# Kernel optimization log

Measured on AMD Instinct MI355X. Metric: run time of the kernel, lower is better.

Reference implementation:

```python
import jax, jax.numpy as jnp
import numpy as np

ALPHA = 0.2
NEG = -9e15
EPS = 1e-5


def _gat(h, adj, W, a, out_features):
    # h: [B,N,Fin], adj: [B,N,N], W: [Fin,Fout], a: [2*Fout,1]
    Wh = jnp.matmul(h, W)                      # [B,N,Fout]
    Wh1 = jnp.matmul(Wh, a[:out_features])     # [B,N,1]
    Wh2 = jnp.matmul(Wh, a[out_features:])     # [B,N,1]
    e = Wh1 + jnp.swapaxes(Wh2, 1, 2)          # [B,N,N]
    e = jax.nn.leaky_relu(e, negative_slope=ALPHA)
    scores = jnp.where(adj > 0, e, NEG)
    att = jax.nn.softmax(scores, axis=1)       # NOTE: dim=1 as in source
    return jnp.matmul(att, Wh)                 # [B,N,Fout]


def _layernorm(x, g, b):
    mu = jnp.mean(x, axis=-1, keepdims=True)
    var = jnp.var(x, axis=-1, keepdims=True)
    return (x - mu) * jax.lax.rsqrt(var + EPS) * g + b


def setup_inputs() -> dict:
    key = jax.random.key(0)
    ks = jax.random.split(key, 8)
    B, N, F, H = 2, 4096, 256, 1024
    x = jax.random.normal(ks[0], (B, N, F), dtype=jnp.float32)
    adj = jax.random.randint(ks[1], (B, N, N), 0, 2, dtype=jnp.int32)
    def xavier(k, shape):
        fan_in, fan_out = shape[0], shape[1]
        lim = np.sqrt(6.0 / (fan_in + fan_out))
        return jax.random.uniform(k, shape, jnp.float32, -lim, lim)
    return {
        "x": x,
        "adj": adj,
        "W1": xavier(ks[2], (F, F)),
        "a1": xavier(ks[3], (2 * F, 1)),
        "W2": xavier(ks[4], (F, F)),
        "a2": xavier(ks[5], (2 * F, 1)),
        "w_ff1": xavier(ks[6], (F, H)) ,
        "b_ff1": jnp.zeros((H,), jnp.float32),
        "w_ff2": xavier(ks[7], (H, F)),
        "b_ff2": jnp.zeros((F,), jnp.float32),
        "g_ln1": jnp.ones((F,), jnp.float32),
        "b_ln1": jnp.zeros((F,), jnp.float32),
        "g_ln2": jnp.ones((F,), jnp.float32),
        "b_ln2": jnp.zeros((F,), jnp.float32),
    }


def reference(x, adj, W1, a1, W2, a2, w_ff1, b_ff1, w_ff2, b_ff2,
              g_ln1, b_ln1, g_ln2, b_ln2):
    Fout = W1.shape[1]
    residual = x
    # dropout is a no-op in eval mode
    h = _gat(x, adj, W1, a1, Fout)          # single head -> cat is identity
    h = _gat(h, adj, W2, a2, W2.shape[1])
    h = _layernorm(residual + h, g_ln1, b_ln1)
    residual2 = h
    ff = jnp.matmul(jax.nn.relu(jnp.matmul(h, w_ff1) + b_ff1), w_ff2) + b_ff2
    return _layernorm(residual2 + ff, g_ln2, b_ln2)
```

## Files before the change

kernel.cpp:

```cpp
#include <hip/hip_runtime.h>
#include <math.h>

#define ALPHA 0.2f
#define NEGV  -9e15f
#define EPSV  1e-5f

constexpr int B_ = 2, N_ = 4096, F_ = 256, H_ = 1024;
constexpr int SPLIT_ = 16;
constexpr int SPLITJ_ = 4;

typedef __attribute__((ext_vector_type(4))) float f32x4;
typedef __attribute__((ext_vector_type(8))) short s16x8;

__device__ __forceinline__ unsigned short f2bf(float f) {
    unsigned u = __builtin_bit_cast(unsigned, f);
    u += 0x7fffu + ((u >> 16) & 1u);
    return (unsigned short)(u >> 16);
}

__global__ __launch_bounds__(256) void transp_all_kernel(
    const float* __restrict__ W1, const float* __restrict__ W2,
    const float* __restrict__ F1s, const float* __restrict__ F2s,
    unsigned short* __restrict__ D1, unsigned short* __restrict__ D2,
    unsigned short* __restrict__ D3, unsigned short* __restrict__ D4,
    float* __restrict__ Zp)
{
    const int mi = blockIdx.z;
    const float* src; unsigned short* dst; int R, Cc;
    if (mi == 0)      { src = W1;  dst = D1; R = 256;  Cc = 256; }
    else if (mi == 1) { src = W2;  dst = D2; R = 256;  Cc = 256; }
    else if (mi == 2) { src = F1s; dst = D3; R = 256;  Cc = 1024; }
    else              { src = F2s; dst = D4; R = 1024; Cc = 256; }
    const int r0 = blockIdx.x * 64, c0 = blockIdx.y * 64;
    const int t = threadIdx.x;

    if (mi == 0 && blockIdx.y >= 4) {
        const int lid = (blockIdx.y - 4) * 16 + blockIdx.x;
        if (lid < 32) {
            const int i = (lid * 256 + t) * 4;
            *(float4*)&Zp[i] = make_float4(0.f, 0.f, 0.f, 0.f);
        }
        return;
    }
    if (r0 >= R || c0 >= Cc) return;

    __shared__ float T[64][65];
    #pragma unroll
    for (int s = 0; s < 4; ++s) {
        const int rr = s * 16 + (t >> 4);
        const int cq = t & 15;
        const float4 v = *(const float4*)&src[(size_t)(r0 + rr) * Cc + c0 + cq * 4];
        T[rr][cq * 4 + 0] = v.x; T[rr][cq * 4 + 1] = v.y;
        T[rr][cq * 4 + 2] = v.z; T[rr][cq * 4 + 3] = v.w;
    }
    __syncthreads();
    #pragma unroll
    for (int s = 0; s < 4; ++s) {
        const int cr = s * 16 + (t >> 4);
        const int rq = t & 15;
        ushort4 o;
        o.x = f2bf(T[rq * 4 + 0][cr]);
        o.y = f2bf(T[rq * 4 + 1][cr]);
        o.z = f2bf(T[rq * 4 + 2][cr]);
        o.w = f2bf(T[rq * 4 + 3][cr]);
        *(ushort4*)&dst[(size_t)(c0 + cr) * R + r0 + rq * 4] = o;
    }
}

__global__ __launch_bounds__(256) void gemm128_kernel(
    const void* __restrict__ Ap, const unsigned short* __restrict__ Wt,
    const float* __restrict__ bias, void* __restrict__ Cp,
    unsigned short* __restrict__ Tout, const float* __restrict__ wha,
    float* __restrict__ Wh1, float* __restrict__ Wh2,
    int Nc, int K, int relu, int a_bf16, int c_mode)
{
    __shared__ unsigned short As[128 * 72];
    __shared__ unsigned short Bs[128 * 72];
    const int t = threadIdx.x;
    const int w = t >> 6, l = t & 63;
    const int quad = l >> 4, l15 = l & 15;
    const int wr = w & 1, wc = w >> 1;
    const int row0 = blockIdx.y * 128, col0 = blockIdx.x * 128;
    const int sr = t >> 1;
    const int sk = (t & 1) * 32;

    f32x4 acc[4][4];
    #pragma unroll
    for (int it = 0; it < 4; ++it)
        #pragma unroll
        for (int ft = 0; ft < 4; ++ft) acc[it][ft] = (f32x4)(0.f);

    for (int k0 = 0; k0 < K; k0 += 64) {
        if (a_bf16) {
            const unsigned short* ap =
                (const unsigned short*)Ap + (size_t)(row0 + sr) * K + k0 + sk;
            #pragma unroll
            for (int u = 0; u < 4; ++u)
                *(s16x8*)&As[sr * 72 + sk + u * 8] = *(const s16x8*)(ap + u * 8);
        } else {
            const float* ap = (const float*)Ap + (size_t)(row0 + sr) * K + k0 + sk;
            #pragma unroll
            for (int u = 0; u < 8; ++u) {
                const float4 v = *(const float4*)(ap + u * 4);
                ushort4 o;
                o.x = f2bf(v.x); o.y = f2bf(v.y); o.z = f2bf(v.z); o.w = f2bf(v.w);
                *(ushort4*)&As[sr * 72 + sk + u * 4] = o;
            }
        }
        {
            const unsigned short* bp = Wt + (size_t)(col0 + sr) * K + k0 + sk;
            #pragma unroll
            for (int u = 0; u < 4; ++u)
                *(s16x8*)&Bs[sr * 72 + sk + u * 8] = *(const s16x8*)(bp + u * 8);
        }
        __syncthreads();
        #pragma unroll
        for (int ks = 0; ks < 64; ks += 32) {
            s16x8 af[4], bf[4];
            #pragma unroll
            for (int it = 0; it < 4; ++it)
                af[it] = *(const s16x8*)&As[(wr * 64 + it * 16 + l15) * 72 + ks + quad * 8];
            #pragma unroll
            for (int ft = 0; ft < 4; ++ft)
                bf[ft] = *(const s16x8*)&Bs[(wc * 64 + ft * 16 + l15) * 72 + ks + quad * 8];
            #pragma unroll
            for (int ft = 0; ft < 4; ++ft)
                #pragma unroll
                for (int it = 0; it < 4; ++it)
                    acc[it][ft] = __builtin_amdgcn_mfma_f32_16x16x32_bf16(
                        af[it], bf[ft], acc[it][ft], 0, 0, 0);
        }
        __syncthreads();
    }

    if (c_mode) {
        #pragma unroll
        for (int ft = 0; ft < 4; ++ft) {
            const int col = col0 + wc * 64 + ft * 16 + l15;
            const float bv = bias ? bias[col] : 0.f;
            #pragma unroll
            for (int it = 0; it < 4; ++it) {
                const int rbase = row0 + wr * 64 + it * 16 + quad * 4;
                #pragma unroll
                for (int rr = 0; rr < 4; ++rr) {
                    float v = acc[it][ft][rr] + bv;
                    if (relu) v = fmaxf(v, 0.f);
                    if (c_mode == 2)
                        ((unsigned short*)Cp)[(size_t)(rbase + rr) * Nc + col] = f2bf(v);
                    else
                        ((float*)Cp)[(size_t)(rbase + rr) * Nc + col] = v;
                }
            }
        }
    }

    if (Tout) {
        const int bb = row0 >> 12;
        #pragma unroll
        for (int ft = 0; ft < 4; ++ft) {
            const int col = col0 + wc * 64 + ft * 16 + l15;
            #pragma unroll
            for (int it = 0; it < 4; ++it) {
                const int ibase = (row0 & (N_ - 1)) + wr * 64 + it * 16 + quad * 4;
                ushort4 o;
                o.x = f2bf(acc[it][ft][0]); o.y = f2bf(acc[it][ft][1]);
                o.z = f2bf(acc[it][ft][2]); o.w = f2bf(acc[it][ft][3]);
                *(ushort4*)&Tout[((size_t)bb * F_ + col) * N_ + ibase] = o;
            }
        }
    }

    if (wha) {
        float a1v[4], a2v[4];
        #pragma unroll
        for (int ft = 0; ft < 4; ++ft) {
            const int col = col0 + wc * 64 + ft * 16 + l15;
            a1v[ft] = wha[col];
            a2v[ft] = wha[F_ + col];
        }
        #pragma unroll
        for (int it = 0; it < 4; ++it)
            #pragma unroll
            for (int rr = 0; rr < 4; ++rr) {
                float s1 = 0.f, s2 = 0.f;
                #pragma unroll
                for (int ft = 0; ft < 4; ++ft) {
                    s1 += acc[it][ft][rr] * a1v[ft];
                    s2 += acc[it][ft][rr] * a2v[ft];
                }
                #pragma unroll
                for (int mkk = 1; mkk < 16; mkk <<= 1) {
                    s1 += __shfl_xor(s1, mkk);
                    s2 += __shfl_xor(s2, mkk);
                }
                if (l15 == 0) {
                    const int row = row0 + wr * 64 + it * 16 + quad * 4 + rr;
                    atomicAdd(&Wh1[row], s1);
                    atomicAdd(&Wh2[row], s2);
                }
            }
    }
}

__global__ __launch_bounds__(256) void gemm64_kernel(
    const void* __restrict__ Ap, const unsigned short* __restrict__ Wt,
    const float* __restrict__ bias, void* __restrict__ Cp,
    unsigned short* __restrict__ Tout, const float* __restrict__ wha,
    float* __restrict__ Wh1, float* __restrict__ Wh2,
    int Nc, int K, int relu, int a_mode, int c_mode)
{
    __shared__ unsigned short As[64 * 72];
    __shared__ unsigned short Bs[128 * 72];
    const int t = threadIdx.x;
    const int w = t >> 6, l = t & 63;
    const int quad = l >> 4, l15 = l & 15;
    const int row0 = blockIdx.y * 64, col0 = blockIdx.x * 128;
    const int sra = t >> 2;
    const int ska = (t & 3) * 16;
    const int srb = t >> 1;
    const int skb = (t & 1) * 32;

    f32x4 acc[4][2];
    #pragma unroll
    for (int it = 0; it < 4; ++it)
        #pragma unroll
        for (int ft = 0; ft < 2; ++ft) acc[it][ft] = (f32x4)(0.f);

    for (int k0 = 0; k0 < K; k0 += 64) {
        if (a_mode == 1) {
            const unsigned short* ap =
                (const unsigned short*)Ap + (size_t)(row0 + sra) * K + k0 + ska;
            *(s16x8*)&As[sra * 72 + ska]     = *(const s16x8*)ap;
            *(s16x8*)&As[sra * 72 + ska + 8] = *(const s16x8*)(ap + 8);
        } else if (a_mode == 0) {
            const float* ap = (const float*)Ap + (size_t)(row0 + sra) * K + k0 + ska;
            #pragma unroll
            for (int u = 0; u < 4; ++u) {
                const float4 v = *(const float4*)(ap + u * 4);
                ushort4 o;
                o.x = f2bf(v.x); o.y = f2bf(v.y); o.z = f2bf(v.z); o.w = f2bf(v.w);
                *(ushort4*)&As[sra * 72 + ska + u * 4] = o;
            }
        } else {
            const size_t S = (size_t)B_ * N_ * F_;
            const float* ap = (const float*)Ap + (size_t)(row0 + sra) * K + k0 + ska;
            #pragma unroll
            for (int u = 0; u < 4; ++u) {
                const float4 a = *(const float4*)(ap + u * 4);
                const float4 b = *(const float4*)(ap + S + u * 4);
                const float4 c = *(const float4*)(ap + 2 * S + u * 4);
                const float4 d = *(const float4*)(ap + 3 * S + u * 4);
                ushort4 o;
                o.x = f2bf(a.x + b.x + c.x + d.x);
                o.y = f2bf(a.y + b.y + c.y + d.y);
                o.z = f2bf(a.z + b.z + c.z + d.z);
                o.w = f2bf(a.w + b.w + c.w + d.w);
                *(ushort4*)&As[sra * 72 + ska + u * 4] = o;
            }
        }
        {
            const unsigned short* bp = Wt + (size_t)(col0 + srb) * K + k0 + skb;
            #pragma unroll
            for (int u = 0; u < 4; ++u)
                *(s16x8*)&Bs[srb * 72 + skb + u * 8] = *(const s16x8*)(bp + u * 8);
        }
        __syncthreads();
        #pragma unroll
        for (int ks = 0; ks < 64; ks += 32) {
            s16x8 af[4], bf[2];
            #pragma unroll
            for (int it = 0; it < 4; ++it)
                af[it] = *(const s16x8*)&As[(it * 16 + l15) * 72 + ks + quad * 8];
            #pragma unroll
            for (int ft = 0; ft < 2; ++ft)
                bf[ft] = *(const s16x8*)&Bs[(w * 32 + ft * 16 + l15) * 72 + ks + quad * 8];
            #pragma unroll
            for (int ft = 0; ft < 2; ++ft)
                #pragma unroll
                for (int it = 0; it < 4; ++it)
                    acc[it][ft] = __builtin_amdgcn_mfma_f32_16x16x32_bf16(
                        af[it], bf[ft], acc[it][ft], 0, 0, 0);
        }
        __syncthreads();
    }

    if (c_mode) {
        #pragma unroll
        for (int ft = 0; ft < 2; ++ft) {
            const int col = col0 + w * 32 + ft * 16 + l15;
            const float bv = bias ? bias[col] : 0.f;
            #pragma unroll
            for (int it = 0; it < 4; ++it) {
                const int rbase = row0 + it * 16 + quad * 4;
                #pragma unroll
                for (int rr = 0; rr < 4; ++rr) {
                    float v = acc[it][ft][rr] + bv;
                    if (relu) v = fmaxf(v, 0.f);
                    if (c_mode == 2)
                        ((unsigned short*)Cp)[(size_t)(rbase + rr) * Nc + col] = f2bf(v);
                    else
                        ((float*)Cp)[(size_t)(rbase + rr) * Nc + col] = v;
                }
            }
        }
    }

    if (Tout) {
        const int bb = row0 >> 12;
        #pragma unroll
        for (int ft = 0; ft < 2; ++ft) {
            const int col = col0 + w * 32 + ft * 16 + l15;
            #pragma unroll
            for (int it = 0; it < 4; ++it) {
                const int ibase = (row0 & (N_ - 1)) + it * 16 + quad * 4;
                ushort4 o;
                o.x = f2bf(acc[it][ft][0]); o.y = f2bf(acc[it][ft][1]);
                o.z = f2bf(acc[it][ft][2]); o.w = f2bf(acc[it][ft][3]);
                *(ushort4*)&Tout[((size_t)bb * F_ + col) * N_ + ibase] = o;
            }
        }
    }

    if (wha) {
        float a1v[2], a2v[2];
        #pragma unroll
        for (int ft = 0; ft < 2; ++ft) {
            const int col = col0 + w * 32 + ft * 16 + l15;
            a1v[ft] = wha[col];
            a2v[ft] = wha[F_ + col];
        }
        #pragma unroll
        for (int it = 0; it < 4; ++it)
            #pragma unroll
            for (int rr = 0; rr < 4; ++rr) {
                float s1 = acc[it][0][rr] * a1v[0] + acc[it][1][rr] * a1v[1];
                float s2 = acc[it][0][rr] * a2v[0] + acc[it][1][rr] * a2v[1];
                #pragma unroll
                for (int mkk = 1; mkk < 16; mkk <<= 1) {
                    s1 += __shfl_xor(s1, mkk);
                    s2 += __shfl_xor(s2, mkk);
                }
                if (l15 == 0) {
                    const int row = row0 + it * 16 + quad * 4 + rr;
                    atomicAdd(&Wh1[row], s1);
                    atomicAdd(&Wh2[row], s2);
                }
            }
    }
}

__global__ __launch_bounds__(256) void colstats_adj_kernel(
    const int* __restrict__ adj, unsigned long long* __restrict__ maskOut,
    const float* __restrict__ Wh1, const float* __restrict__ Wh2,
    float* __restrict__ pM, float* __restrict__ pS)
{
    const int t = threadIdx.x;
    const int j = blockIdx.x * 256 + t;
    const int sp = blockIdx.y;
    const int b = blockIdx.z;
    const int i0 = sp * (N_ / SPLIT_);
    const int w = t >> 6, l = t & 63;
    const float w2 = Wh2[b * N_ + j];
    const float* __restrict__ w1p = Wh1 + b * N_ + i0;
    const int* __restrict__ ap = adj + ((size_t)b * N_ + i0) * N_ + j;

    float m = -3.4e38f, s = 0.f;
    for (int c = 0; c < N_ / SPLIT_; c += 8) {
        int v[8];
        #pragma unroll
        for (int u = 0; u < 8; ++u) v[u] = ap[(size_t)(c + u) * N_];
        float x[8];
        #pragma unroll
        for (int u = 0; u < 8; ++u) {
            const bool act = v[u] > 0;
            const unsigned long long bm = __ballot(act);
            if (l == 0)
                maskOut[((size_t)b * N_ + i0 + c + u) * (N_ / 64) + blockIdx.x * 4 + w] = bm;
            const float e0 = w1p[c + u] + w2;
            const float e = fmaxf(e0, ALPHA * e0);
            x[u] = act ? e : NEGV;
        }
        const float cm = fmaxf(fmaxf(fmaxf(x[0], x[1]), fmaxf(x[2], x[3])),
                               fmaxf(fmaxf(x[4], x[5]), fmaxf(x[6], x[7])));
        const float nm = fmaxf(m, cm);
        float cs = 0.f;
        #pragma unroll
        for (int u = 0; u < 8; ++u) cs += __expf(x[u] - nm);
        s = s * __expf(m - nm) + cs;
        m = nm;
    }
    pM[((size_t)b * SPLIT_ + sp) * N_ + j] = m;
    pS[((size_t)b * SPLIT_ + sp) * N_ + j] = s;
}

__global__ __launch_bounds__(256) void colstats3_kernel(
    const unsigned long long* __restrict__ mask,
    const float* __restrict__ Wh1, const float* __restrict__ Wh2,
    float* __restrict__ pM, float* __restrict__ pS)
{
    const int t = threadIdx.x;
    const int j = blockIdx.x * 256 + t;
    const int sp = blockIdx.y;
    const int b = blockIdx.z;
    const int i0 = sp * (N_ / SPLIT_);
    const int w = t >> 6;
    const int jbit = t & 63;
    const float w2 = Wh2[b * N_ + j];
    const unsigned long long* __restrict__ mbase =
        mask + ((size_t)b * N_ + i0) * (N_ / 64) + blockIdx.x * 4 + w;
    const float* __restrict__ w1p = Wh1 + b * N_ + i0;

    float m = -3.4e38f, s = 0.f;
    for (int c = 0; c < N_ / SPLIT_; c += 8) {
        float x[8];
        #pragma unroll
        for (int u = 0; u < 8; ++u) {
            const unsigned long long mw = mbase[(size_t)(c + u) * (N_ / 64)];
            const float e0 = w1p[c + u] + w2;
            const float e = fmaxf(e0, ALPHA * e0);
            x[u] = ((mw >> jbit) & 1ull) ? e : NEGV;
        }
        const float cm = fmaxf(fmaxf(fmaxf(x[0], x[1]), fmaxf(x[2], x[3])),
                               fmaxf(fmaxf(x[4], x[5]), fmaxf(x[6], x[7])));
        const float nm = fmaxf(m, cm);
        float cs = 0.f;
        #pragma unroll
        for (int u = 0; u < 8; ++u) cs += __expf(x[u] - nm);
        s = s * __expf(m - nm) + cs;
        m = nm;
    }
    pM[((size_t)b * SPLIT_ + sp) * N_ + j] = m;
    pS[((size_t)b * SPLIT_ + sp) * N_ + j] = s;
}

__global__ __launch_bounds__(256) void colfin2_kernel(
    const float* __restrict__ pM, const float* __restrict__ pS,
    float* __restrict__ Mo)
{
    const int j = blockIdx.x * 256 + threadIdx.x;
    const int b = blockIdx.y;
    float m = -3.4e38f;
    #pragma unroll
    for (int s = 0; s < SPLIT_; ++s)
        m = fmaxf(m, pM[((size_t)b * SPLIT_ + s) * N_ + j]);
    float sum = 0.f;
    #pragma unroll
    for (int s = 0; s < SPLIT_; ++s)
        sum += pS[((size_t)b * SPLIT_ + s) * N_ + j] *
               __expf(pM[((size_t)b * SPLIT_ + s) * N_ + j] - m);
    Mo[b * N_ + j] = m + logf(sum);
}

__global__ __launch_bounds__(256, 2) void att_mfma4_kernel(
    const unsigned short* __restrict__ mask16, const unsigned short* __restrict__ Wht,
    const float* __restrict__ Wh1, const float* __restrict__ Wh2,
    const float* __restrict__ Mo, float* __restrict__ part)
{
    __shared__ unsigned short Ps[2][64 * 72];
    __shared__ float w2s[1024];
    __shared__ float mos[1024];

    const int t = threadIdx.x;
    const int w = t >> 6, l = t & 63;
    const int quad = l >> 4, l15 = l & 15;

    const int lin = blockIdx.x + (blockIdx.y << 6) + (blockIdx.z << 8);
    const int xcd = lin & 7;
    const int b = xcd >> 2;
    const int sp = xcd & 3;
    const int i0 = (lin >> 3) << 6;
    const int jbase = sp * (N_ / SPLITJ_);

    const int pi = t >> 2;
    const int pj4 = t & 3;
    const float w1i = Wh1[b * N_ + i0 + pi];
    const unsigned short* __restrict__ mrow =
        mask16 + ((size_t)b * N_ + i0 + pi) * (N_ / 16) + pj4;
    const unsigned short* __restrict__ WhtB = Wht + (size_t)b * F_ * N_;

    {
        const float4 a = *(const float4*)&Wh2[b * N_ + jbase + t * 4];
        const float4 c = *(const float4*)&Mo[b * N_ + jbase + t * 4];
        *(float4*)&w2s[t * 4] = a;
        *(float4*)&mos[t * 4] = c;
    }

    f32x4 acc[4][4];
    #pragma unroll
    for (int it = 0; it < 4; ++it)
        #pragma unroll
        for (int ft = 0; ft < 4; ++ft) acc[it][ft] = (f32x4)(0.f);

    const unsigned short* __restrict__ bbase =
        WhtB + (size_t)(w * 64 + l15) * N_ + jbase + quad * 8;

    s16x8 bA[8], bB[8];

    auto prefB = [&](int itr2, s16x8* dst) {
        const unsigned short* nb = bbase + itr2 * 64;
        #pragma unroll
        for (int ft = 0; ft < 4; ++ft)
            #pragma unroll
            for (int kk = 0; kk < 2; ++kk)
                dst[ft * 2 + kk] = *(const s16x8*)&nb[(size_t)ft * 16 * N_ + kk * 32];
    };

    auto computeP = [&](int itr2, unsigned short* psdst) {
        const int jl = itr2 * 64 + pj4 * 16;
        const unsigned mb = mrow[(jbase >> 4) + itr2 * 4];
        s16x8 o0, o1;
        #pragma unroll
        for (int u4 = 0; u4 < 4; ++u4) {
            const float4 w2v = *(const float4*)&w2s[jl + u4 * 4];
            const float4 mov = *(const float4*)&mos[jl + u4 * 4];
            #pragma unroll
            for (int u = 0; u < 4; ++u) {
                const float xw = w1i + (&w2v.x)[u];
                const float e = fmaxf(xw, ALPHA * xw);
                const float x2 = ((mb >> (u4 * 4 + u)) & 1u) ? e : NEGV;
                const short pv = (short)f2bf(__expf(x2 - (&mov.x)[u]));
                if (u4 < 2) o0[u4 * 4 + u] = pv;
                else        o1[(u4 - 2) * 4 + u] = pv;
            }
        }
        *(s16x8*)&psdst[pi * 72 + pj4 * 16]     = o0;
        *(s16x8*)&psdst[pi * 72 + pj4 * 16 + 8] = o1;
    };

    auto mfmaStep = [&](const unsigned short* ps, const s16x8* breg) {
        #pragma unroll
        for (int ksidx = 0; ksidx < 2; ++ksidx) {
            s16x8 af[4];
            #pragma unroll
            for (int it = 0; it < 4; ++it)
                af[it] = *(const s16x8*)&ps[(it * 16 + l15) * 72 + ksidx * 32 + quad * 8];
            #pragma unroll
            for (int ft = 0; ft < 4; ++ft)
                #pragma unroll
                for (int it = 0; it < 4; ++it)
                    acc[it][ft] = __builtin_amdgcn_mfma_f32_16x16x32_bf16(
                        af[it], breg[ft * 2 + ksidx], acc[it][ft], 0, 0, 0);
        }
    };

    prefB(0, bA);
    __syncthreads();
    computeP(0, &Ps[0][0]);
    __syncthreads();

    constexpr int NITER = (N_ / SPLITJ_) / 64;
    for (int itr = 0; itr < NITER; itr += 2) {
        prefB(itr + 1, bB);
        computeP(itr + 1, &Ps[1][0]);
        mfmaStep(&Ps[0][0], bA);
        __syncthreads();
        if (itr + 2 < NITER) {
            prefB(itr + 2, bA);
            computeP(itr + 2, &Ps[0][0]);
        }
        mfmaStep(&Ps[1][0], bB);
        __syncthreads();
    }

    float* __restrict__ pout = part + ((size_t)sp * B_ + b) * N_ * F_;
    #pragma unroll
    for (int it = 0; it < 4; ++it)
        #pragma unroll
        for (int ft = 0; ft < 4; ++ft) {
            const int col = w * 64 + ft * 16 + l15;
            #pragma unroll
            for (int rr = 0; rr < 4; ++rr) {
                const int row = i0 + it * 16 + quad * 4 + rr;
                pout[(size_t)row * F_ + col] = acc[it][ft][rr];
            }
        }
}

__global__ __launch_bounds__(256) void addln4_kernel(
    const float* __restrict__ X, const float* __restrict__ p,
    const float* __restrict__ g, const float* __restrict__ bta,
    float* __restrict__ outf, unsigned short* __restrict__ outb)
{
    const int row = blockIdx.x;
    const int t = threadIdx.x;
    const size_t idx = (size_t)row * F_ + t;
    const size_t S = (size_t)B_ * N_ * F_;
    const float v = X[idx] + p[idx] + p[idx + S] + p[idx + 2 * S] + p[idx + 3 * S];
    float s1 = v, s2 = v * v;
    #pragma unroll
    for (int off = 32; off > 0; off >>= 1) {
        s1 += __shfl_down(s1, off);
        s2 += __shfl_down(s2, off);
    }
    __shared__ float r1[4], r2[4];
    __shared__ float mu_s, rs_s;
    const int wid = t >> 6, lane = t & 63;
    if (lane == 0) { r1[wid] = s1; r2[wid] = s2; }
    __syncthreads();
    if (t == 0) {
        const float a = r1[0] + r1[1] + r1[2] + r1[3];
        const float q = r2[0] + r2[1] + r2[2] + r2[3];
        const float mu = a * (1.f / F_);
        const float var = q * (1.f / F_) - mu * mu;
        mu_s = mu;
        rs_s = rsqrtf(var + EPSV);
    }
    __syncthreads();
    const float r = (v - mu_s) * rs_s * g[t] + bta[t];
    outf[idx] = r;
    outb[idx] = f2bf(r);
}

__global__ __launch_bounds__(256) void addln_kernel(
    const float* __restrict__ X, const float* __restrict__ Y,
    const float* __restrict__ g, const float* __restrict__ bta,
    float* __restrict__ out)
{
    const int row = blockIdx.x;
    const int t = threadIdx.x;
    const size_t idx = (size_t)row * F_ + t;
    const float v = X[idx] + Y[idx];
    float s1 = v, s2 = v * v;
    #pragma unroll
    for (int off = 32; off > 0; off >>= 1) {
        s1 += __shfl_down(s1, off);
        s2 += __shfl_down(s2, off);
    }
    __shared__ float r1[4], r2[4];
    __shared__ float mu_s, rs_s;
    const int wid = t >> 6, lane = t & 63;
    if (lane == 0) { r1[wid] = s1; r2[wid] = s2; }
    __syncthreads();
    if (t == 0) {
        const float a = r1[0] + r1[1] + r1[2] + r1[3];
        const float q = r2[0] + r2[1] + r2[2] + r2[3];
        const float mu = a * (1.f / F_);
        const float var = q * (1.f / F_) - mu * mu;
        mu_s = mu;
        rs_s = rsqrtf(var + EPSV);
    }
    __syncthreads();
    out[idx] = (v - mu_s) * rs_s * g[t] + bta[t];
}

extern "C" void kernel_launch(void* const* d_in, const int* in_sizes, int n_in,
                              void* d_out, int out_size, void* d_ws, size_t ws_size,
                              hipStream_t stream)
{
    const float* x     = (const float*)d_in[0];
    const int*   adj   = (const int*)d_in[1];
    const float* W1    = (const float*)d_in[2];
    const float* a1    = (const float*)d_in[3];
    const float* W2    = (const float*)d_in[4];
    const float* a2    = (const float*)d_in[5];
    const float* w_ff1 = (const float*)d_in[6];
    const float* b_ff1 = (const float*)d_in[7];
    const float* w_ff2 = (const float*)d_in[8];
    const float* b_ff2 = (const float*)d_in[9];
    const float* g_ln1 = (const float*)d_in[10];
    const float* b_ln1 = (const float*)d_in[11];
    const float* g_ln2 = (const float*)d_in[12];
    const float* b_ln2 = (const float*)d_in[13];
    float* out = (float*)d_out;

    const int Rtot = B_ * N_;
    char* wsb = (char*)d_ws;
    float* part  = (float*)wsb;
    float* ln1   = (float*)(wsb + 33554432);
    float* ffout = (float*)(wsb + 41943040);
    unsigned short* mid  = (unsigned short*)(wsb + 50331648);
    unsigned short* ln1b = (unsigned short*)(wsb + 67108864);
    unsigned short* Wht  = (unsigned short*)(wsb + 75497472);
    unsigned long long* mask = (unsigned long long*)(wsb + 79691776);
    unsigned short* mask16 = (unsigned short*)mask;
    unsigned short* Wt1  = (unsigned short*)(wsb + 83886080);
    unsigned short* Wt2  = Wt1 + 65536;
    unsigned short* Wtf1 = Wt2 + 65536;
    unsigned short* Wtf2 = Wtf1 + 262144;
    float* WhA1 = (float*)(wsb + 85196800);
    float* WhA2 = WhA1 + 8192;
    float* WhB1 = WhA2 + 8192;
    float* WhB2 = WhB1 + 8192;
    float* Mo   = (float*)(wsb + 85327872);
    float* pM   = (float*)(wsb + 85360640);
    float* pS   = (float*)(wsb + 85884928);

    const dim3 statsG(N_ / 256, SPLIT_, B_);
    const dim3 finG(N_ / 256, B_);
    const dim3 attG(N_ / 64, SPLITJ_, B_);

    transp_all_kernel<<<dim3(16, 16, 4), 256, 0, stream>>>(
        W1, W2, w_ff1, w_ff2, Wt1, Wt2, Wtf1, Wtf2, WhA1);

    gemm64_kernel<<<dim3(2, 128), 256, 0, stream>>>(
        x, Wt1, nullptr, nullptr, Wht, a1, WhA1, WhA2, F_, F_, 0, 0, 0);
    colstats_adj_kernel<<<statsG, 256, 0, stream>>>(adj, mask, WhA1, WhA2, pM, pS);
    colfin2_kernel<<<finG, 256, 0, stream>>>(pM, pS, Mo);
    att_mfma4_kernel<<<attG, 256, 0, stream>>>(mask16, Wht, WhA1, WhA2, Mo, part);

    gemm64_kernel<<<dim3(2, 128), 256, 0, stream>>>(
        part, Wt2, nullptr, nullptr, Wht, a2, WhB1, WhB2, F_, F_, 0, 2, 0);
    colstats3_kernel<<<statsG, 256, 0, stream>>>(mask, WhB1, WhB2, pM, pS);
    colfin2_kernel<<<finG, 256, 0, stream>>>(pM, pS, Mo);
    att_mfma4_kernel<<<attG, 256, 0, stream>>>(mask16, Wht, WhB1, WhB2, Mo, part);

    addln4_kernel<<<Rtot, 256, 0, stream>>>(x, part, g_ln1, b_ln1, ln1, ln1b);

    gemm128_kernel<<<dim3(8, 64), 256, 0, stream>>>(
        ln1b, Wtf1, b_ff1, mid, nullptr, nullptr, nullptr, nullptr, H_, F_, 1, 1, 2);
    gemm64_kernel<<<dim3(2, 128), 256, 0, stream>>>(
        mid, Wtf2, b_ff2, ffout, nullptr, nullptr, nullptr, nullptr, F_, H_, 0, 1, 1);

    addln_kernel<<<Rtot, 256, 0, stream>>>(ln1, ffout, g_ln2, b_ln2, out);
}
```

Measured before the change: 425.8 us.

## Halve GEMM row tiles and use 512-thread attention blocks with smaller per-wave tiles

The 64-row GEMM becomes a 32-row tile kernel launched on twice as many blocks, which raises block count for the small N=256 GEMMs. The attention kernel moves from 256 to 512 threads. Each of its 8 waves now covers 32 output columns instead of 64, cutting accumulator and prefetch registers so that more waves fit per CU. The P-tile construction is split across 8 threads per row, each extracting its own mask byte. The cost is reloading the mask and probability tiles for twice as many waves, and reloading the B operand per smaller tile.

```diff
diff --git a/kernel.cpp b/kernel.cpp
--- a/kernel.cpp
+++ b/kernel.cpp
@@ -202,27 +202,27 @@
     }
 }
 
-__global__ __launch_bounds__(256) void gemm64_kernel(
+__global__ __launch_bounds__(256) void gemm32_kernel(
     const void* __restrict__ Ap, const unsigned short* __restrict__ Wt,
     const float* __restrict__ bias, void* __restrict__ Cp,
     unsigned short* __restrict__ Tout, const float* __restrict__ wha,
     float* __restrict__ Wh1, float* __restrict__ Wh2,
     int Nc, int K, int relu, int a_mode, int c_mode)
 {
-    __shared__ unsigned short As[64 * 72];
+    __shared__ unsigned short As[32 * 72];
     __shared__ unsigned short Bs[128 * 72];
     const int t = threadIdx.x;
     const int w = t >> 6, l = t & 63;
     const int quad = l >> 4, l15 = l & 15;
-    const int row0 = blockIdx.y * 64, col0 = blockIdx.x * 128;
-    const int sra = t >> 2;
-    const int ska = (t & 3) * 16;
+    const int row0 = blockIdx.y * 32, col0 = blockIdx.x * 128;
+    const int sra = t >> 3;
+    const int ska = (t & 7) * 8;
     const int srb = t >> 1;
     const int skb = (t & 1) * 32;
 
-    f32x4 acc[4][2];
-    #pragma unroll
-    for (int it = 0; it < 4; ++it)
+    f32x4 acc[2][2];
+    #pragma unroll
+    for (int it = 0; it < 2; ++it)
         #pragma unroll
         for (int ft = 0; ft < 2; ++ft) acc[it][ft] = (f32x4)(0.f);
 
@@ -230,12 +230,11 @@
         if (a_mode == 1) {
             const unsigned short* ap =
                 (const unsigned short*)Ap + (size_t)(row0 + sra) * K + k0 + ska;
-            *(s16x8*)&As[sra * 72 + ska]     = *(const s16x8*)ap;
-            *(s16x8*)&As[sra * 72 + ska + 8] = *(const s16x8*)(ap + 8);
+            *(s16x8*)&As[sra * 72 + ska] = *(const s16x8*)ap;
         } else if (a_mode == 0) {
             const float* ap = (const float*)Ap + (size_t)(row0 + sra) * K + k0 + ska;
             #pragma unroll
-            for (int u = 0; u < 4; ++u) {
+            for (int u = 0; u < 2; ++u) {
                 const float4 v = *(const float4*)(ap + u * 4);
                 ushort4 o;
                 o.x = f2bf(v.x); o.y = f2bf(v.y); o.z = f2bf(v.z); o.w = f2bf(v.w);
@@ -245,7 +244,7 @@
             const size_t S = (size_t)B_ * N_ * F_;
             const float* ap = (const float*)Ap + (size_t)(row0 + sra) * K + k0 + ska;
             #pragma unroll
-            for (int u = 0; u < 4; ++u) {
+            for (int u = 0; u < 2; ++u) {
                 const float4 a = *(const float4*)(ap + u * 4);
                 const float4 b = *(const float4*)(ap + S + u * 4);
                 const float4 c = *(const float4*)(ap + 2 * S + u * 4);
@@ -267,9 +266,9 @@
         __syncthreads();
         #pragma unroll
         for (int ks = 0; ks < 64; ks += 32) {
-            s16x8 af[4], bf[2];
-            #pragma unroll
-            for (int it = 0; it < 4; ++it)
+            s16x8 af[2], bf[2];
+            #pragma unroll
+            for (int it = 0; it < 2; ++it)
                 af[it] = *(const s16x8*)&As[(it * 16 + l15) * 72 + ks + quad * 8];
             #pragma unroll
             for (int ft = 0; ft < 2; ++ft)
@@ -277,7 +276,7 @@
             #pragma unroll
             for (int ft = 0; ft < 2; ++ft)
                 #pragma unroll
-                for (int it = 0; it < 4; ++it)
+                for (int it = 0; it < 2; ++it)
                     acc[it][ft] = __builtin_amdgcn_mfma_f32_16x16x32_bf16(
                         af[it], bf[ft], acc[it][ft], 0, 0, 0);
         }
@@ -290,7 +289,7 @@
             const int col = col0 + w * 32 + ft * 16 + l15;
             const float bv = bias ? bias[col] : 0.f;
             #pragma unroll
-            for (int it = 0; it < 4; ++it) {
+            for (int it = 0; it < 2; ++it) {
                 const int rbase = row0 + it * 16 + quad * 4;
                 #pragma unroll
                 for (int rr = 0; rr < 4; ++rr) {
@@ -311,7 +310,7 @@
         for (int ft = 0; ft < 2; ++ft) {
             const int col = col0 + w * 32 + ft * 16 + l15;
             #pragma unroll
-            for (int it = 0; it < 4; ++it) {
+            for (int it = 0; it < 2; ++it) {
                 const int ibase = (row0 & (N_ - 1)) + it * 16 + quad * 4;
                 ushort4 o;
                 o.x = f2bf(acc[it][ft][0]); o.y = f2bf(acc[it][ft][1]);
@@ -330,7 +329,7 @@
             a2v[ft] = wha[F_ + col];
         }
         #pragma unroll
-        for (int it = 0; it < 4; ++it)
+        for (int it = 0; it < 2; ++it)
             #pragma unroll
             for (int rr = 0; rr < 4; ++rr) {
                 float s1 = acc[it][0][rr] * a1v[0] + acc[it][1][rr] * a1v[1];
@@ -451,7 +450,7 @@
     Mo[b * N_ + j] = m + logf(sum);
 }
 
-__global__ __launch_bounds__(256, 2) void att_mfma4_kernel(
+__global__ __launch_bounds__(512, 4) void att_mfma7_kernel(
     const unsigned short* __restrict__ mask16, const unsigned short* __restrict__ Wht,
     const float* __restrict__ Wh1, const float* __restrict__ Wh2,
     const float* __restrict__ Mo, float* __restrict__ part)
@@ -471,46 +470,47 @@
     const int i0 = (lin >> 3) << 6;
     const int jbase = sp * (N_ / SPLITJ_);
 
-    const int pi = t >> 2;
-    const int pj4 = t & 3;
+    const int pi = t >> 3;
+    const int pj8 = t & 7;
     const float w1i = Wh1[b * N_ + i0 + pi];
     const unsigned short* __restrict__ mrow =
-        mask16 + ((size_t)b * N_ + i0 + pi) * (N_ / 16) + pj4;
+        mask16 + ((size_t)b * N_ + i0 + pi) * (N_ / 16);
     const unsigned short* __restrict__ WhtB = Wht + (size_t)b * F_ * N_;
 
-    {
+    if (t < 256) {
         const float4 a = *(const float4*)&Wh2[b * N_ + jbase + t * 4];
         const float4 c = *(const float4*)&Mo[b * N_ + jbase + t * 4];
         *(float4*)&w2s[t * 4] = a;
         *(float4*)&mos[t * 4] = c;
     }
 
-    f32x4 acc[4][4];
+    f32x4 acc[4][2];
     #pragma unroll
     for (int it = 0; it < 4; ++it)
         #pragma unroll
-        for (int ft = 0; ft < 4; ++ft) acc[it][ft] = (f32x4)(0.f);
+        for (int ft = 0; ft < 2; ++ft) acc[it][ft] = (f32x4)(0.f);
 
     const unsigned short* __restrict__ bbase =
-        WhtB + (size_t)(w * 64 + l15) * N_ + jbase + quad * 8;
-
-    s16x8 bA[8], bB[8];
+        WhtB + (size_t)(w * 32 + l15) * N_ + jbase + quad * 8;
+
+    s16x8 bA[4], bB[4];
 
     auto prefB = [&](int itr2, s16x8* dst) {
         const unsigned short* nb = bbase + itr2 * 64;
         #pragma unroll
-        for (int ft = 0; ft < 4; ++ft)
+        for (int ft = 0; ft < 2; ++ft)
             #pragma unroll
             for (int kk = 0; kk < 2; ++kk)
                 dst[ft * 2 + kk] = *(const s16x8*)&nb[(size_t)ft * 16 * N_ + kk * 32];
     };
 
     auto computeP = [&](int itr2, unsigned short* psdst) {
-        const int jl = itr2 * 64 + pj4 * 16;
-        const unsigned mb = mrow[(jbase >> 4) + itr2 * 4];
-        s16x8 o0, o1;
-        #pragma unroll
-        for (int u4 = 0; u4 < 4; ++u4) {
+        const unsigned mword = mrow[(jbase >> 4) + itr2 * 4 + (pj8 >> 1)];
+        const unsigned mb = (mword >> ((pj8 & 1) * 8)) & 0xffu;
+        const int jl = itr2 * 64 + pj8 * 8;
+        s16x8 o;
+        #pragma unroll
+        for (int u4 = 0; u4 < 2; ++u4) {
             const float4 w2v = *(const float4*)&w2s[jl + u4 * 4];
             const float4 mov = *(const float4*)&mos[jl + u4 * 4];
             #pragma unroll
@@ -518,13 +518,10 @@
                 const float xw = w1i + (&w2v.x)[u];
                 const float e = fmaxf(xw, ALPHA * xw);
                 const float x2 = ((mb >> (u4 * 4 + u)) & 1u) ? e : NEGV;
-                const short pv = (short)f2bf(__expf(x2 - (&mov.x)[u]));
-                if (u4 < 2) o0[u4 * 4 + u] = pv;
-                else        o1[(u4 - 2) * 4 + u] = pv;
-            }
-        }
-        *(s16x8*)&psdst[pi * 72 + pj4 * 16]     = o0;
-        *(s16x8*)&psdst[pi * 72 + pj4 * 16 + 8] = o1;
+                o[u4 * 4 + u] = (short)f2bf(__expf(x2 - (&mov.x)[u]));
+            }
+        }
+        *(s16x8*)&psdst[pi * 72 + pj8 * 8] = o;
     };
 
     auto mfmaStep = [&](const unsigned short* ps, const s16x8* breg) {
@@ -535,7 +532,7 @@
             for (int it = 0; it < 4; ++it)
                 af[it] = *(const s16x8*)&ps[(it * 16 + l15) * 72 + ksidx * 32 + quad * 8];
             #pragma unroll
-            for (int ft = 0; ft < 4; ++ft)
+            for (int ft = 0; ft < 2; ++ft)
                 #pragma unroll
                 for (int it = 0; it < 4; ++it)
                     acc[it][ft] = __builtin_amdgcn_mfma_f32_16x16x32_bf16(
@@ -566,8 +563,8 @@
     #pragma unroll
     for (int it = 0; it < 4; ++it)
         #pragma unroll
-        for (int ft = 0; ft < 4; ++ft) {
-            const int col = w * 64 + ft * 16 + l15;
+        for (int ft = 0; ft < 2; ++ft) {
+            const int col = w * 32 + ft * 16 + l15;
             #pragma unroll
             for (int rr = 0; rr < 4; ++rr) {
                 const int row = i0 + it * 16 + quad * 4 + rr;
@@ -692,23 +689,23 @@
     transp_all_kernel<<<dim3(16, 16, 4), 256, 0, stream>>>(
         W1, W2, w_ff1, w_ff2, Wt1, Wt2, Wtf1, Wtf2, WhA1);
 
-    gemm64_kernel<<<dim3(2, 128), 256, 0, stream>>>(
+    gemm32_kernel<<<dim3(2, 256), 256, 0, stream>>>(
         x, Wt1, nullptr, nullptr, Wht, a1, WhA1, WhA2, F_, F_, 0, 0, 0);
     colstats_adj_kernel<<<statsG, 256, 0, stream>>>(adj, mask, WhA1, WhA2, pM, pS);
     colfin2_kernel<<<finG, 256, 0, stream>>>(pM, pS, Mo);
-    att_mfma4_kernel<<<attG, 256, 0, stream>>>(mask16, Wht, WhA1, WhA2, Mo, part);
-
-    gemm64_kernel<<<dim3(2, 128), 256, 0, stream>>>(
+    att_mfma7_kernel<<<attG, 512, 0, stream>>>(mask16, Wht, WhA1, WhA2, Mo, part);
+
+    gemm32_kernel<<<dim3(2, 256), 256, 0, stream>>>(
         part, Wt2, nullptr, nullptr, Wht, a2, WhB1, WhB2, F_, F_, 0, 2, 0);
     colstats3_kernel<<<statsG, 256, 0, stream>>>(mask, WhB1, WhB2, pM, pS);
     colfin2_kernel<<<finG, 256, 0, stream>>>(pM, pS, Mo);
-    att_mfma4_kernel<<<attG, 256, 0, stream>>>(mask16, Wht, WhB1, WhB2, Mo, part);
+    att_mfma7_kernel<<<attG, 512, 0, stream>>>(mask16, Wht, WhB1, WhB2, Mo, part);
 
     addln4_kernel<<<Rtot, 256, 0, stream>>>(x, part, g_ln1, b_ln1, ln1, ln1b);
 
     gemm128_kernel<<<dim3(8, 64), 256, 0, stream>>>(
         ln1b, Wtf1, b_ff1, mid, nullptr, nullptr, nullptr, nullptr, H_, F_, 1, 1, 2);
-    gemm64_kernel<<<dim3(2, 128), 256, 0, stream>>>(
+    gemm32_kernel<<<dim3(2, 256), 256, 0, stream>>>(
         mid, Wtf2, b_ff2, ffout, nullptr, nullptr, nullptr, nullptr, F_, H_, 0, 1, 1);
 
     addln_kernel<<<Rtot, 256, 0, stream>>>(ln1, ffout, g_ln2, b_ln2, out);
```

Measured after the change: 418.3 us. No clear change (-1.8%).
